# Performance work log

Measured on AMD Instinct MI355X. Metric: run time of the kernel, lower is better.

Reference implementation:

```python
import jax, jax.numpy as jnp
import numpy as np

N_NODES = 100000
N_EDGES = 3200000
IN_DIM = 256
OUT_DIM = 64


def setup_inputs() -> dict:
    key = jax.random.key(0)
    k1, k2, k3 = jax.random.split(key, 3)
    h = jax.random.normal(k1, (N_NODES, IN_DIM), dtype=jnp.float32)
    W = jax.random.normal(k2, (IN_DIM, OUT_DIM), dtype=jnp.float32) * (IN_DIM ** -0.5)
    b = jnp.zeros((OUT_DIM,), dtype=jnp.float32)
    edges = jax.random.randint(k3, (2, N_EDGES), 0, N_NODES, dtype=jnp.int64)
    return {"h": h, "W": W, "b": b, "edges": edges}


def reference(h, W, b, edges):
    # DGL GraphConv, norm='both':
    #   out = D_dst^{-1/2} * A * (D_src^{-1/2} * (h @ W)) + b
    # degrees clamped to min 1; then log_softmax over classes.
    N = h.shape[0]
    src, dst = edges[0], edges[1]
    ones = jnp.ones(src.shape, dtype=h.dtype)
    out_deg = jax.ops.segment_sum(ones, src, num_segments=N)
    in_deg = jax.ops.segment_sum(ones, dst, num_segments=N)
    norm_src = jnp.maximum(out_deg, 1.0) ** -0.5  # [N]
    norm_dst = jnp.maximum(in_deg, 1.0) ** -0.5   # [N]
    # in_dim > out_dim: project first (matches DGL's mult-first optimization)
    m = (h @ W) * norm_src[:, None]               # [N, out_dim]
    agg = jax.ops.segment_sum(m[src], dst, num_segments=N)  # SpMM
    out = agg * norm_dst[:, None] + b
    return jax.nn.log_softmax(out, axis=1)
```

## Files before the change

kernel.cpp:

```cpp
#include <hip/hip_runtime.h>
#include <hip/hip_fp16.h>
#include <math.h>

#define IN_DIM 256
#define OUT_DIM 64
#define BROWS 256
#define GROWS 128
#define SC_THREADS 512
#define SC_EPB 16
#define SC_EDGES (SC_THREADS * SC_EPB)
#define BM 128
#define KC2 64
#define LDH 68
#define CSR_CAP 5120

typedef _Float16 f16x4 __attribute__((ext_vector_type(4)));
typedef float f32x4 __attribute__((ext_vector_type(4)));

__global__ void __launch_bounds__(SC_THREADS) scatter_pairs_kernel(
        const int* __restrict__ src, const int* __restrict__ dst,
        int* __restrict__ dcursor, int* __restrict__ scursor,
        unsigned* __restrict__ pairs, unsigned char* __restrict__ sbytes,
        int n_edges, int nb, int cap) {
    __shared__ int lhd[512];
    __shared__ int lbd[512];
    __shared__ int lod[512];
    __shared__ int lhs[512];
    __shared__ int lbs[512];
    __shared__ int los[512];
    __shared__ unsigned stp[SC_EDGES];
    __shared__ unsigned char stb[SC_EDGES];

    const int t = threadIdx.x;
    const int wave = t >> 6;
    const int lane = t & 63;

    lhd[t] = 0; lhs[t] = 0;
    __syncthreads();

    const int base = blockIdx.x * SC_EDGES;
    int s[SC_EPB], d[SC_EPB];
    if (base + SC_EDGES <= n_edges) {
        const int4* s4 = (const int4*)(src + base);
        const int4* d4 = (const int4*)(dst + base);
        #pragma unroll
        for (int j = 0; j < SC_EPB / 4; ++j) {
            int4 a = s4[j * SC_THREADS + t];
            int4 c = d4[j * SC_THREADS + t];
            s[4*j+0] = a.x; s[4*j+1] = a.y; s[4*j+2] = a.z; s[4*j+3] = a.w;
            d[4*j+0] = c.x; d[4*j+1] = c.y; d[4*j+2] = c.z; d[4*j+3] = c.w;
        }
        #pragma unroll
        for (int i = 0; i < SC_EPB; ++i) {
            atomicAdd(&lhd[d[i] >> 8], 1);
            atomicAdd(&lhs[s[i] >> 8], 1);
        }
    } else {
        #pragma unroll
        for (int i = 0; i < SC_EPB; ++i) {
            int e = base + i * SC_THREADS + t;
            if (e < n_edges) {
                s[i] = src[e];
                d[i] = dst[e];
                atomicAdd(&lhd[d[i] >> 8], 1);
                atomicAdd(&lhs[s[i] >> 8], 1);
            } else {
                s[i] = -1; d[i] = 0;
            }
        }
    }
    __syncthreads();

    for (int i = t; i < nb; i += SC_THREADS) {
        int c = lhd[i];
        lbd[i] = c ? atomicAdd(&dcursor[i], c) : 0;
        c = lhs[i];
        lbs[i] = c ? atomicAdd(&scursor[i], c) : 0;
    }

    {
        int vd = (t < nb) ? lhd[t] : 0;
        int vs = (t < nb) ? lhs[t] : 0;
        lod[t] = vd; los[t] = vs;
        __syncthreads();
        #pragma unroll
        for (int dd = 1; dd < 512; dd <<= 1) {
            int td = (t >= dd) ? lod[t - dd] : 0;
            int ts = (t >= dd) ? los[t - dd] : 0;
            __syncthreads();
            lod[t] += td; los[t] += ts;
            __syncthreads();
        }
        lod[t] -= vd; los[t] -= vs;
    }
    __syncthreads();

    #pragma unroll
    for (int i = 0; i < SC_EPB; ++i) {
        if (s[i] >= 0) {
            int bkt = d[i] >> 8;
            int pos = atomicAdd(&lod[bkt], 1);
            stp[pos] = ((unsigned)s[i] << 8) | (unsigned)(d[i] & 255);
            int sb = s[i] >> 8;
            int spos = atomicAdd(&los[sb], 1);
            stb[spos] = (unsigned char)(s[i] & 255);
        }
    }
    __syncthreads();

    for (int b2 = wave; b2 < nb; b2 += SC_THREADS / 64) {
        int cnt = lhd[b2];
        if (cnt) {
            int st = lod[b2] - cnt;
            int gb = lbd[b2];
            unsigned* gp = pairs + (size_t)b2 * cap;
            for (int j = lane; j < cnt; j += 64)
                if (gb + j < cap) gp[gb + j] = stp[st + j];
        }
        cnt = lhs[b2];
        if (cnt) {
            int st = los[b2] - cnt;
            int gb = lbs[b2];
            unsigned char* gp = sbytes + (size_t)b2 * cap;
            for (int j = lane; j < cnt; j += 64)
                if (gb + j < cap) gp[gb + j] = stb[st + j];
        }
    }
}

__global__ void __launch_bounds__(256) count_src_kernel(
        const unsigned char* __restrict__ sbytes, const int* __restrict__ scursor,
        int* __restrict__ out_deg, int n_nodes, int cap) {
    __shared__ int cnt[BROWS];
    cnt[threadIdx.x] = 0;
    __syncthreads();
    const int beg = blockIdx.x * cap;
    int len = scursor[blockIdx.x];
    if (len > cap) len = cap;
    const int end = beg + len;
    for (int i = beg + threadIdx.x; i < end; i += 256)
        atomicAdd(&cnt[sbytes[i]], 1);
    __syncthreads();
    const int row = blockIdx.x * BROWS + threadIdx.x;
    if (row < n_nodes) out_deg[row] = cnt[threadIdx.x];
}

__global__ void __launch_bounds__(256) gemm_kernel(
        const float* __restrict__ h, const float* __restrict__ W,
        const int* __restrict__ out_deg, __half* __restrict__ m, int n_nodes) {
    __shared__ _Float16 hs[BM * LDH];
    __shared__ _Float16 Wt[OUT_DIM * LDH];

    const int t = threadIdx.x;
    const int wave = t >> 6;
    const int lane = t & 63;
    const int lg = lane >> 4;
    const int li = lane & 15;
    const int rowBase = blockIdx.x * BM;

    f32x4 acc[2][4];
    #pragma unroll
    for (int rt = 0; rt < 2; ++rt)
        #pragma unroll
        for (int ct = 0; ct < 4; ++ct)
            acc[rt][ct] = (f32x4){0.f, 0.f, 0.f, 0.f};

    for (int kc = 0; kc < IN_DIM / KC2; ++kc) {
        __syncthreads();
        #pragma unroll
        for (int i = 0; i < 8; ++i) {
            int idx = t + 256 * i;
            int row = idx >> 4;
            int s4 = idx & 15;
            float4 v = make_float4(0.f, 0.f, 0.f, 0.f);
            if (rowBase + row < n_nodes)
                v = *(const float4*)(h + (size_t)(rowBase + row) * IN_DIM
                                     + kc * KC2 + s4 * 4);
            _Float16* dp = &hs[row * LDH + s4 * 4];
            dp[0] = (_Float16)v.x; dp[1] = (_Float16)v.y;
            dp[2] = (_Float16)v.z; dp[3] = (_Float16)v.w;
        }
        #pragma unroll
        for (int i = 0; i < 16; ++i) {
            int idx = t + 256 * i;
            int k = idx >> 6;
            int n = idx & 63;
            Wt[n * LDH + k] = (_Float16)W[(size_t)(kc * KC2 + k) * OUT_DIM + n];
        }
        __syncthreads();

        #pragma unroll
        for (int ks = 0; ks < KC2 / 16; ++ks) {
            const int k0 = ks * 16 + lg * 4;
            f16x4 b0 = *(const f16x4*)&hs[((wave * 2 + 0) * 16 + li) * LDH + k0];
            f16x4 b1 = *(const f16x4*)&hs[((wave * 2 + 1) * 16 + li) * LDH + k0];
            f16x4 a0 = *(const f16x4*)&Wt[(0 * 16 + li) * LDH + k0];
            f16x4 a1 = *(const f16x4*)&Wt[(1 * 16 + li) * LDH + k0];
            f16x4 a2 = *(const f16x4*)&Wt[(2 * 16 + li) * LDH + k0];
            f16x4 a3 = *(const f16x4*)&Wt[(3 * 16 + li) * LDH + k0];
            acc[0][0] = __builtin_amdgcn_mfma_f32_16x16x16f16(a0, b0, acc[0][0], 0, 0, 0);
            acc[0][1] = __builtin_amdgcn_mfma_f32_16x16x16f16(a1, b0, acc[0][1], 0, 0, 0);
            acc[0][2] = __builtin_amdgcn_mfma_f32_16x16x16f16(a2, b0, acc[0][2], 0, 0, 0);
            acc[0][3] = __builtin_amdgcn_mfma_f32_16x16x16f16(a3, b0, acc[0][3], 0, 0, 0);
            acc[1][0] = __builtin_amdgcn_mfma_f32_16x16x16f16(a0, b1, acc[1][0], 0, 0, 0);
            acc[1][1] = __builtin_amdgcn_mfma_f32_16x16x16f16(a1, b1, acc[1][1], 0, 0, 0);
            acc[1][2] = __builtin_amdgcn_mfma_f32_16x16x16f16(a2, b1, acc[1][2], 0, 0, 0);
            acc[1][3] = __builtin_amdgcn_mfma_f32_16x16x16f16(a3, b1, acc[1][3], 0, 0, 0);
        }
    }

    #pragma unroll
    for (int rt = 0; rt < 2; ++rt) {
        int row = rowBase + (wave * 2 + rt) * 16 + li;
        if (row < n_nodes) {
            float nr = rsqrtf(fmaxf((float)out_deg[row], 1.0f));
            #pragma unroll
            for (int ct = 0; ct < 4; ++ct) {
                f32x4 dv = acc[rt][ct];
                union { __half2 h2[2]; uint2 u; } pk;
                pk.h2[0] = __floats2half2_rn(dv[0] * nr, dv[1] * nr);
                pk.h2[1] = __floats2half2_rn(dv[2] * nr, dv[3] * nr);
                *(uint2*)(m + (size_t)row * OUT_DIM + ct * 16 + lg * 4) = pk.u;
            }
        }
    }
}

__global__ void __launch_bounds__(512) bucket_gather_kernel(
        const unsigned* __restrict__ pairs, const int* __restrict__ dcursor,
        const __half* __restrict__ m, const float* __restrict__ b,
        float* __restrict__ out, int n_nodes, int cap) {
    __shared__ int cnt[GROWS];
    __shared__ int rofs[GROWS];
    __shared__ int cur[GROWS];
    __shared__ int csr[CSR_CAP];

    const int t = threadIdx.x;
    const int bkt = blockIdx.x >> 1;
    const int hsel = blockIdx.x & 1;
    const unsigned hbit = (unsigned)hsel << 7;
    const int beg = bkt * cap;
    int len = dcursor[bkt];
    if (len > cap) len = cap;
    const int end = beg + len;
    const int rowBase = bkt * BROWS + hsel * GROWS;

    const int wave = t >> 6;
    const int lane = t & 63;
    const int half = lane >> 5;
    const int c    = lane & 31;
    const __half2* __restrict__ m2 = (const __half2*)m;
    const float2 bb = *(const float2*)(b + 2 * c);

    if (t < GROWS) cnt[t] = 0;
    __syncthreads();

    for (int i = beg + t; i < end; i += 512) {
        unsigned p = pairs[i];
        if ((p & 128u) == hbit) atomicAdd(&cnt[p & 127u], 1);
    }
    __syncthreads();
    if (t < GROWS) rofs[t] = cnt[t];
    __syncthreads();
    #pragma unroll
    for (int d = 1; d < GROWS; d <<= 1) {
        int tv = (t < GROWS && t >= d) ? rofs[t - d] : 0;
        __syncthreads();
        if (t < GROWS) rofs[t] += tv;
        __syncthreads();
    }
    if (t < GROWS) cur[t] = rofs[t] - cnt[t];
    __syncthreads();
    const int tot = rofs[GROWS - 1];

    if (tot <= CSR_CAP) {
        for (int i = beg + t; i < end; i += 512) {
            unsigned p = pairs[i];
            if ((p & 128u) == hbit) {
                int pos = atomicAdd(&cur[p & 127u], 1);
                csr[pos] = (int)(p >> 8);
            }
        }
        __syncthreads();
        #pragma unroll 1
        for (int p8 = 0; p8 < GROWS / 16; ++p8) {
            const int rA = wave + 16 * p8;
            const int rB = rA + 8;
            const int eA = rofs[rA]; const int bAe = eA - cnt[rA];
            const int eB = rofs[rB]; const int bBe = eB - cnt[rB];
            float axA = 0.f, ayA = 0.f, axB = 0.f, ayB = 0.f;
            int iA = bAe, iB = bBe;
            while (iA + 16 <= eA && iB + 16 <= eB) {
                int sA[8], sB[8];
                #pragma unroll
                for (int k = 0; k < 8; ++k) sA[k] = csr[iA + 2 * k + half];
                #pragma unroll
                for (int k = 0; k < 8; ++k) sB[k] = csr[iB + 2 * k + half];
                float2 fA[8], fB[8];
                #pragma unroll
                for (int k = 0; k < 8; ++k)
                    fA[k] = __half22float2(m2[(unsigned)(sA[k] * (OUT_DIM / 2) + c)]);
                #pragma unroll
                for (int k = 0; k < 8; ++k)
                    fB[k] = __half22float2(m2[(unsigned)(sB[k] * (OUT_DIM / 2) + c)]);
                #pragma unroll
                for (int k = 0; k < 8; ++k) {
                    axA += fA[k].x; ayA += fA[k].y;
                    axB += fB[k].x; ayB += fB[k].y;
                }
                iA += 16; iB += 16;
            }
            for (; iA + 16 <= eA; iA += 16) {
                int s[8];
                #pragma unroll
                for (int k = 0; k < 8; ++k) s[k] = csr[iA + 2 * k + half];
                float2 f[8];
                #pragma unroll
                for (int k = 0; k < 8; ++k)
                    f[k] = __half22float2(m2[(unsigned)(s[k] * (OUT_DIM / 2) + c)]);
                #pragma unroll
                for (int k = 0; k < 8; ++k) { axA += f[k].x; ayA += f[k].y; }
            }
            for (int e = iA + half; e < eA; e += 2) {
                float2 f = __half22float2(m2[(unsigned)(csr[e] * (OUT_DIM / 2) + c)]);
                axA += f.x; ayA += f.y;
            }
            for (; iB + 16 <= eB; iB += 16) {
                int s[8];
                #pragma unroll
                for (int k = 0; k < 8; ++k) s[k] = csr[iB + 2 * k + half];
                float2 f[8];
                #pragma unroll
                for (int k = 0; k < 8; ++k)
                    f[k] = __half22float2(m2[(unsigned)(s[k] * (OUT_DIM / 2) + c)]);
                #pragma unroll
                for (int k = 0; k < 8; ++k) { axB += f[k].x; ayB += f[k].y; }
            }
            for (int e = iB + half; e < eB; e += 2) {
                float2 f = __half22float2(m2[(unsigned)(csr[e] * (OUT_DIM / 2) + c)]);
                axB += f.x; ayB += f.y;
            }
            #pragma unroll
            for (int which = 0; which < 2; ++which) {
                float ax = which ? axB : axA;
                float ay = which ? ayB : ayA;
                const int r = which ? rB : rA;
                const int row = rowBase + r;
                ax += __shfl_xor(ax, 32, 64);
                ay += __shfl_xor(ay, 32, 64);
                float nd = rsqrtf(fmaxf((float)cnt[r], 1.0f));
                float x0 = ax * nd + bb.x;
                float x1 = ay * nd + bb.y;
                float mx = fmaxf(x0, x1);
                #pragma unroll
                for (int o = 16; o > 0; o >>= 1) mx = fmaxf(mx, __shfl_xor(mx, o, 64));
                float ex0 = expf(x0 - mx), ex1 = expf(x1 - mx);
                float sm = ex0 + ex1;
                #pragma unroll
                for (int o = 16; o > 0; o >>= 1) sm += __shfl_xor(sm, o, 64);
                float ls = logf(sm);
                if (half == 0 && row < n_nodes)
                    *(float2*)(out + (size_t)row * OUT_DIM + 2 * c) =
                        make_float2(x0 - mx - ls, x1 - mx - ls);
            }
        }
    } else {
        for (int r = wave; r < GROWS; r += 8) {
            const int row = rowBase + r;
            if (row >= n_nodes) continue;
            const unsigned match = (unsigned)(hsel * GROWS + r);
            float ax = 0.f, ay = 0.f;
            for (int e = beg; e < end; ++e) {
                unsigned p = pairs[e];
                if ((p & 255u) == match) {
                    float2 f = __half22float2(m2[(unsigned)((p >> 8) * (OUT_DIM / 2) + c)]);
                    ax += f.x; ay += f.y;
                }
            }
            float nd = rsqrtf(fmaxf((float)cnt[r], 1.0f));
            float x0 = ax * nd + bb.x;
            float x1 = ay * nd + bb.y;
            float mx = fmaxf(x0, x1);
            #pragma unroll
            for (int o = 16; o > 0; o >>= 1) mx = fmaxf(mx, __shfl_xor(mx, o, 64));
            float ex0 = expf(x0 - mx), ex1 = expf(x1 - mx);
            float sm = ex0 + ex1;
            #pragma unroll
            for (int o = 16; o > 0; o >>= 1) sm += __shfl_xor(sm, o, 64);
            float ls = logf(sm);
            if (half == 0)
                *(float2*)(out + (size_t)row * OUT_DIM + 2 * c) =
                    make_float2(x0 - mx - ls, x1 - mx - ls);
        }
    }
}

static inline size_t align16(size_t x) { return (x + 15) & ~(size_t)15; }

extern "C" void kernel_launch(void* const* d_in, const int* in_sizes, int n_in,
                              void* d_out, int out_size, void* d_ws, size_t ws_size,
                              hipStream_t stream) {
    const float* h = (const float*)d_in[0];
    const float* W = (const float*)d_in[1];
    const float* b = (const float*)d_in[2];
    const int* edges = (const int*)d_in[3];

    const int out_dim = in_sizes[2];
    const int in_dim  = in_sizes[1] / out_dim;
    const int n_nodes = in_sizes[0] / in_dim;
    const int n_edges = in_sizes[3] / 2;

    const int* src = edges;
    const int* dst = edges + n_edges;

    float* out = (float*)d_out;

    const int nb = (n_nodes + BROWS - 1) / BROWS;

    const int epb = (n_edges + nb - 1) / nb;
    const int cap = (epb + (epb >> 2) + 1023 + 1023) & ~1023;

    char* ws = (char*)d_ws;
    size_t off = 0;
    int* out_deg     = (int*)(ws + off); off = align16(off + (size_t)n_nodes * 4);
    int* dcursor     = (int*)(ws + off); off = align16(off + (size_t)nb * 4);
    int* scursor     = (int*)(ws + off); off = align16(off + (size_t)nb * 4);
    __half* m        = (__half*)(ws + off); off = align16(off + (size_t)n_nodes * OUT_DIM * 2);
    unsigned* pairs  = (unsigned*)(ws + off); off = align16(off + (size_t)nb * cap * 4);
    unsigned char* sbytes = (unsigned char*)m;

    (void)hipMemsetAsync(dcursor, 0,
                         (size_t)((char*)(scursor + nb) - (char*)dcursor), stream);

    const int sc_blocks = (n_edges + SC_EDGES - 1) / SC_EDGES;

    scatter_pairs_kernel<<<sc_blocks, SC_THREADS, 0, stream>>>(
        src, dst, dcursor, scursor, pairs, sbytes, n_edges, nb, cap);
    count_src_kernel<<<nb, 256, 0, stream>>>(sbytes, scursor, out_deg, n_nodes, cap);

    gemm_kernel<<<(n_nodes + BM - 1) / BM, 256, 0, stream>>>(h, W, out_deg, m, n_nodes);

    bucket_gather_kernel<<<2 * nb, 512, 0, stream>>>(pairs, dcursor, m, b, out,
                                                     n_nodes, cap);
}
```

Before: 358.4 us.

## Fuse source-degree counting into GEMM kernel and halve scatter edges per block

Removes the separate count_src kernel: each GEMM block now counts out-degrees for its 128 rows from the source-byte bucket in shared memory before the matmul, selecting its half of the 256-row bucket by the byte's high bit. The sbytes buffer gets its own workspace region instead of aliasing m, because m is now written by the same kernel that reads sbytes. This drops one launch and the out_deg global round trip, but each bucket's bytes are read twice, once by each of two GEMM blocks. SC_EPB is also halved, which doubles the number of scatter blocks.

```diff
diff --git a/kernel.cpp b/kernel.cpp
--- a/kernel.cpp
+++ b/kernel.cpp
@@ -7,7 +7,7 @@
 #define BROWS 256
 #define GROWS 128
 #define SC_THREADS 512
-#define SC_EPB 16
+#define SC_EPB 8
 #define SC_EDGES (SC_THREADS * SC_EPB)
 #define BM 128
 #define KC2 64
@@ -128,28 +128,13 @@
     }
 }
 
-__global__ void __launch_bounds__(256) count_src_kernel(
-        const unsigned char* __restrict__ sbytes, const int* __restrict__ scursor,
-        int* __restrict__ out_deg, int n_nodes, int cap) {
-    __shared__ int cnt[BROWS];
-    cnt[threadIdx.x] = 0;
-    __syncthreads();
-    const int beg = blockIdx.x * cap;
-    int len = scursor[blockIdx.x];
-    if (len > cap) len = cap;
-    const int end = beg + len;
-    for (int i = beg + threadIdx.x; i < end; i += 256)
-        atomicAdd(&cnt[sbytes[i]], 1);
-    __syncthreads();
-    const int row = blockIdx.x * BROWS + threadIdx.x;
-    if (row < n_nodes) out_deg[row] = cnt[threadIdx.x];
-}
-
 __global__ void __launch_bounds__(256) gemm_kernel(
         const float* __restrict__ h, const float* __restrict__ W,
-        const int* __restrict__ out_deg, __half* __restrict__ m, int n_nodes) {
+        const unsigned char* __restrict__ sbytes, const int* __restrict__ scursor,
+        __half* __restrict__ m, int n_nodes, int cap) {
     __shared__ _Float16 hs[BM * LDH];
     __shared__ _Float16 Wt[OUT_DIM * LDH];
+    __shared__ int cnt[GROWS];
 
     const int t = threadIdx.x;
     const int wave = t >> 6;
@@ -157,6 +142,20 @@
     const int lg = lane >> 4;
     const int li = lane & 15;
     const int rowBase = blockIdx.x * BM;
+
+    {
+        const int bkt = blockIdx.x >> 1;
+        const int hsel = blockIdx.x & 1;
+        int len = scursor[bkt];
+        if (len > cap) len = cap;
+        const unsigned char* sb = sbytes + (size_t)bkt * cap;
+        if (t < GROWS) cnt[t] = 0;
+        __syncthreads();
+        for (int i = t; i < len; i += 256) {
+            int v = sb[i];
+            if ((v >> 7) == hsel) atomicAdd(&cnt[v & 127], 1);
+        }
+    }
 
     f32x4 acc[2][4];
     #pragma unroll
@@ -211,9 +210,10 @@
 
     #pragma unroll
     for (int rt = 0; rt < 2; ++rt) {
-        int row = rowBase + (wave * 2 + rt) * 16 + li;
+        int lrow = (wave * 2 + rt) * 16 + li;
+        int row = rowBase + lrow;
         if (row < n_nodes) {
-            float nr = rsqrtf(fmaxf((float)out_deg[row], 1.0f));
+            float nr = rsqrtf(fmaxf((float)cnt[lrow], 1.0f));
             #pragma unroll
             for (int ct = 0; ct < 4; ++ct) {
                 f32x4 dv = acc[rt][ct];
@@ -422,12 +422,11 @@
 
     char* ws = (char*)d_ws;
     size_t off = 0;
-    int* out_deg     = (int*)(ws + off); off = align16(off + (size_t)n_nodes * 4);
-    int* dcursor     = (int*)(ws + off); off = align16(off + (size_t)nb * 4);
-    int* scursor     = (int*)(ws + off); off = align16(off + (size_t)nb * 4);
-    __half* m        = (__half*)(ws + off); off = align16(off + (size_t)n_nodes * OUT_DIM * 2);
-    unsigned* pairs  = (unsigned*)(ws + off); off = align16(off + (size_t)nb * cap * 4);
-    unsigned char* sbytes = (unsigned char*)m;
+    int* dcursor          = (int*)(ws + off); off = align16(off + (size_t)nb * 4);
+    int* scursor          = (int*)(ws + off); off = align16(off + (size_t)nb * 4);
+    __half* m             = (__half*)(ws + off); off = align16(off + (size_t)n_nodes * OUT_DIM * 2);
+    unsigned* pairs       = (unsigned*)(ws + off); off = align16(off + (size_t)nb * cap * 4);
+    unsigned char* sbytes = (unsigned char*)(ws + off); off = align16(off + (size_t)nb * cap);
 
     (void)hipMemsetAsync(dcursor, 0,
                          (size_t)((char*)(scursor + nb) - (char*)dcursor), stream);
@@ -436,9 +435,9 @@
 
     scatter_pairs_kernel<<<sc_blocks, SC_THREADS, 0, stream>>>(
         src, dst, dcursor, scursor, pairs, sbytes, n_edges, nb, cap);
-    count_src_kernel<<<nb, 256, 0, stream>>>(sbytes, scursor, out_deg, n_nodes, cap);
-
-    gemm_kernel<<<(n_nodes + BM - 1) / BM, 256, 0, stream>>>(h, W, out_deg, m, n_nodes);
+
+    gemm_kernel<<<(n_nodes + BM - 1) / BM, 256, 0, stream>>>(
+        h, W, sbytes, scursor, m, n_nodes, cap);
 
     bucket_gather_kernel<<<2 * nb, 512, 0, stream>>>(pairs, dcursor, m, b, out,
                                                      n_nodes, cap);
```

Measured after the change: 386.0 us. 1.08x slower.

## Count source degrees with direct global atomics instead of bucketed byte scatter

Applied to the files above, without the earlier changes.

Out-degrees are now counted by atomically incrementing out_deg[src] in global memory inside the scatter kernel. This replaces the shared-memory source histogram, prefix scan, byte staging, bucketed byte writes and the separate count_src kernel. The memset now clears out_deg together with the dst cursors. The cost moves to 3.2M global atomics spread across 100k addresses, which may contend in L2. In return it removes a kernel launch, a scan and a round trip through the byte buffer.

```diff
diff --git a/kernel.cpp b/kernel.cpp
--- a/kernel.cpp
+++ b/kernel.cpp
@@ -19,23 +19,19 @@
 
 __global__ void __launch_bounds__(SC_THREADS) scatter_pairs_kernel(
         const int* __restrict__ src, const int* __restrict__ dst,
-        int* __restrict__ dcursor, int* __restrict__ scursor,
-        unsigned* __restrict__ pairs, unsigned char* __restrict__ sbytes,
+        int* __restrict__ dcursor, int* __restrict__ out_deg,
+        unsigned* __restrict__ pairs,
         int n_edges, int nb, int cap) {
     __shared__ int lhd[512];
     __shared__ int lbd[512];
     __shared__ int lod[512];
-    __shared__ int lhs[512];
-    __shared__ int lbs[512];
-    __shared__ int los[512];
     __shared__ unsigned stp[SC_EDGES];
-    __shared__ unsigned char stb[SC_EDGES];
 
     const int t = threadIdx.x;
     const int wave = t >> 6;
     const int lane = t & 63;
 
-    lhd[t] = 0; lhs[t] = 0;
+    lhd[t] = 0;
     __syncthreads();
 
     const int base = blockIdx.x * SC_EDGES;
@@ -53,7 +49,7 @@
         #pragma unroll
         for (int i = 0; i < SC_EPB; ++i) {
             atomicAdd(&lhd[d[i] >> 8], 1);
-            atomicAdd(&lhs[s[i] >> 8], 1);
+            atomicAdd(&out_deg[s[i]], 1);
         }
     } else {
         #pragma unroll
@@ -63,7 +59,7 @@
                 s[i] = src[e];
                 d[i] = dst[e];
                 atomicAdd(&lhd[d[i] >> 8], 1);
-                atomicAdd(&lhs[s[i] >> 8], 1);
+                atomicAdd(&out_deg[s[i]], 1);
             } else {
                 s[i] = -1; d[i] = 0;
             }
@@ -74,24 +70,20 @@
     for (int i = t; i < nb; i += SC_THREADS) {
         int c = lhd[i];
         lbd[i] = c ? atomicAdd(&dcursor[i], c) : 0;
-        c = lhs[i];
-        lbs[i] = c ? atomicAdd(&scursor[i], c) : 0;
     }
 
     {
         int vd = (t < nb) ? lhd[t] : 0;
-        int vs = (t < nb) ? lhs[t] : 0;
-        lod[t] = vd; los[t] = vs;
+        lod[t] = vd;
         __syncthreads();
         #pragma unroll
         for (int dd = 1; dd < 512; dd <<= 1) {
             int td = (t >= dd) ? lod[t - dd] : 0;
-            int ts = (t >= dd) ? los[t - dd] : 0;
             __syncthreads();
-            lod[t] += td; los[t] += ts;
+            lod[t] += td;
             __syncthreads();
         }
-        lod[t] -= vd; los[t] -= vs;
+        lod[t] -= vd;
     }
     __syncthreads();
 
@@ -101,9 +93,6 @@
             int bkt = d[i] >> 8;
             int pos = atomicAdd(&lod[bkt], 1);
             stp[pos] = ((unsigned)s[i] << 8) | (unsigned)(d[i] & 255);
-            int sb = s[i] >> 8;
-            int spos = atomicAdd(&los[sb], 1);
-            stb[spos] = (unsigned char)(s[i] & 255);
         }
     }
     __syncthreads();
@@ -117,32 +106,7 @@
             for (int j = lane; j < cnt; j += 64)
                 if (gb + j < cap) gp[gb + j] = stp[st + j];
         }
-        cnt = lhs[b2];
-        if (cnt) {
-            int st = los[b2] - cnt;
-            int gb = lbs[b2];
-            unsigned char* gp = sbytes + (size_t)b2 * cap;
-            for (int j = lane; j < cnt; j += 64)
-                if (gb + j < cap) gp[gb + j] = stb[st + j];
-        }
-    }
-}
-
-__global__ void __launch_bounds__(256) count_src_kernel(
-        const unsigned char* __restrict__ sbytes, const int* __restrict__ scursor,
-        int* __restrict__ out_deg, int n_nodes, int cap) {
-    __shared__ int cnt[BROWS];
-    cnt[threadIdx.x] = 0;
-    __syncthreads();
-    const int beg = blockIdx.x * cap;
-    int len = scursor[blockIdx.x];
-    if (len > cap) len = cap;
-    const int end = beg + len;
-    for (int i = beg + threadIdx.x; i < end; i += 256)
-        atomicAdd(&cnt[sbytes[i]], 1);
-    __syncthreads();
-    const int row = blockIdx.x * BROWS + threadIdx.x;
-    if (row < n_nodes) out_deg[row] = cnt[threadIdx.x];
+    }
 }
 
 __global__ void __launch_bounds__(256) gemm_kernel(
@@ -424,21 +388,19 @@
     size_t off = 0;
     int* out_deg     = (int*)(ws + off); off = align16(off + (size_t)n_nodes * 4);
     int* dcursor     = (int*)(ws + off); off = align16(off + (size_t)nb * 4);
-    int* scursor     = (int*)(ws + off); off = align16(off + (size_t)nb * 4);
     __half* m        = (__half*)(ws + off); off = align16(off + (size_t)n_nodes * OUT_DIM * 2);
     unsigned* pairs  = (unsigned*)(ws + off); off = align16(off + (size_t)nb * cap * 4);
-    unsigned char* sbytes = (unsigned char*)m;
-
-    (void)hipMemsetAsync(dcursor, 0,
-                         (size_t)((char*)(scursor + nb) - (char*)dcursor), stream);
+
+    (void)hipMemsetAsync(out_deg, 0,
+                         (size_t)((char*)(dcursor + nb) - (char*)out_deg), stream);
 
     const int sc_blocks = (n_edges + SC_EDGES - 1) / SC_EDGES;
 
     scatter_pairs_kernel<<<sc_blocks, SC_THREADS, 0, stream>>>(
-        src, dst, dcursor, scursor, pairs, sbytes, n_edges, nb, cap);
-    count_src_kernel<<<nb, 256, 0, stream>>>(sbytes, scursor, out_deg, n_nodes, cap);
-
-    gemm_kernel<<<(n_nodes + BM - 1) / BM, 256, 0, stream>>>(h, W, out_deg, m, n_nodes);
+        src, dst, dcursor, out_deg, pairs, n_edges, nb, cap);
+
+    gemm_kernel<<<(n_nodes + BM - 1) / BM, 256, 0, stream>>>(
+        h, W, out_deg, m, n_nodes);
 
     bucket_gather_kernel<<<2 * nb, 512, 0, stream>>>(pairs, dcursor, m, b, out,
                                                      n_nodes, cap);
```

Measured after the change: 447.2 us. 24.8% more time.
